# Kernel optimization log

Hardware: AMD Instinct MI355X
Metric: run time of the kernel (lower is better)

The kernel has to match this reference:

```python
import jax, jax.numpy as jnp
import numpy as np

B, IC, H, W = 1024, 3, 32, 32
E, NC = 8, 100            # num_experts, num_classes
GCH, ECH = 16, 32         # gate hidden channels, expert hidden channels
K = 3                     # conv kernel size


def _conv2d(x, w):
    # x: [B,Cin,H,W], w: [Cout,Cin,kh,kw] -> [B,Cout,H,W] (SAME padding, stride 1)
    return jax.lax.conv_general_dilated(
        x, w, window_strides=(1, 1), padding='SAME',
        dimension_numbers=('NCHW', 'OIHW', 'NCHW'))


def setup_inputs() -> dict:
    key = jax.random.key(0)
    ks = jax.random.split(key, 9)
    init = lambda k, shape, fan: (jax.random.normal(k, shape, jnp.float32)
                                  * np.float32(1.0 / np.sqrt(fan)))
    return {
        'x': jax.random.normal(ks[0], (B, IC, H, W), jnp.float32),
        # GatingNetwork: conv(3->16) + relu + global-avg-pool + linear(16->E) + softmax
        'gate_conv_w': init(ks[1], (GCH, IC, K, K), IC * K * K),
        'gate_conv_b': jnp.zeros((GCH,), jnp.float32),
        'gate_lin_w': init(ks[2], (E, GCH), GCH),
        'gate_lin_b': jnp.zeros((E,), jnp.float32),
        # ExpertLayer (per expert): conv(3->32) + relu + global-avg-pool + linear(32->NC)
        'exp_conv_w': init(ks[3], (E, ECH, IC, K, K), IC * K * K),
        'exp_conv_b': jnp.zeros((E, ECH), jnp.float32),
        'exp_lin_w': init(ks[4], (E, NC, ECH), ECH),
        'exp_lin_b': jnp.zeros((E, NC), jnp.float32),
    }


def reference(x, gate_conv_w, gate_conv_b, gate_lin_w, gate_lin_b,
              exp_conv_w, exp_conv_b, exp_lin_w, exp_lin_b):
    # ---- Router: softmax gate over experts ----
    g = jax.nn.relu(_conv2d(x, gate_conv_w) + gate_conv_b[None, :, None, None])
    g = g.mean(axis=(2, 3))                                   # [B,GCH]
    weights = jax.nn.softmax(g @ gate_lin_w.T + gate_lin_b, axis=1)  # [B,E]
    best = jnp.argmax(weights, axis=1)                        # [B] hard top-1

    # ---- All experts as one fused conv (dense compute, then hard select) ----
    e, ch, ic, kh, kw = exp_conv_w.shape
    w_all = exp_conv_w.reshape(e * ch, ic, kh, kw)
    feat = _conv2d(x, w_all)                                  # [B,E*ECH,H,W]
    feat = feat.reshape(x.shape[0], e, ch, feat.shape[2], feat.shape[3])
    feat = jax.nn.relu(feat + exp_conv_b[None, :, :, None, None])
    pooled = feat.mean(axis=(3, 4))                           # [B,E,ECH]
    out_all = jnp.einsum('bec,enc->ben', pooled, exp_lin_w) + exp_lin_b[None]  # [B,E,NC]

    # Combine: each row gets only its argmax expert's output (others -> zero grad)
    final = jnp.take_along_axis(out_all, best[:, None, None], axis=1)[:, 0, :]  # [B,NC]
    return (final, weights)
```

## Files before the change

kernel.cpp:

```cpp
#include <hip/hip_runtime.h>
#include <math.h>

#define NB 1024
#define IC 3
#define HW 32
#define GCH 16
#define ECH 32
#define NE 8
#define NC 100

#define RS 38
#define PS 1292
#define NTX 3876

typedef __attribute__((ext_vector_type(8))) short bf16x8;
typedef __attribute__((ext_vector_type(4))) int   int4v;
typedef __attribute__((ext_vector_type(4))) float f32x4;

__device__ inline short f2bf(float f) {
    unsigned u = __float_as_uint(f);
    unsigned r = (u + 0x7FFF + ((u >> 16) & 1)) >> 16;
    return (short)r;
}
__device__ inline float bf2f(short h) {
    return __uint_as_float(((unsigned)(unsigned short)h) << 16);
}

__global__ __launch_bounds__(256) void moe_fused_kernel(
    const float* __restrict__ x,
    const float* __restrict__ gcw,
    const float* __restrict__ gcb,
    const float* __restrict__ glw,
    const float* __restrict__ glb,
    const float* __restrict__ ecw,
    const float* __restrict__ ecb,
    const float* __restrict__ elw,
    const float* __restrict__ elb,
    float* __restrict__ out_final,
    float* __restrict__ out_w)
{
    __shared__ __align__(16) int xil[NTX];
    __shared__ float red2[4][32];
    __shared__ float pg[GCH];
    __shared__ float pe[ECH];
    __shared__ int s_best;

    const int t = threadIdx.x;
    const int b = blockIdx.x;
    const int lane = t & 63;
    const int wid = t >> 6;
    const int r15 = lane & 15;
    const int kg = lane >> 4;

    for (int i = t; i < NTX / 4; i += 256) ((int4*)xil)[i] = make_int4(0, 0, 0, 0);

    bf16x8 gbh, gbl;
    #pragma unroll
    for (int r = 0; r < 8; ++r) {
        int k = kg * 8 + r;
        float w = (k < 27) ? gcw[r15 * 27 + k] : 0.f;
        short h = f2bf(w);
        gbh[r] = h;
        gbl[r] = f2bf(w - bf2f(h));
    }
    const float gb = gcb[r15];

    __syncthreads();

    const float* xb = x + (size_t)b * (IC * HW * HW);
    #pragma unroll
    for (int i3 = 0; i3 < 3; ++i3) {
        int i = t + i3 * 256;
        float4 v = ((const float4*)xb)[i];
        int ci = i >> 8, rem = i & 255, row = rem >> 3, x4 = (rem & 7) << 2;
        int T = ci * PS + (row + 1) * RS + x4 + 2;
        short h0 = f2bf(v.x), h1 = f2bf(v.y), h2 = f2bf(v.z), h3 = f2bf(v.w);
        int t0 = (unsigned short)h0 | ((unsigned)(unsigned short)f2bf(v.x - bf2f(h0)) << 16);
        int t1 = (unsigned short)h1 | ((unsigned)(unsigned short)f2bf(v.y - bf2f(h1)) << 16);
        int t2 = (unsigned short)h2 | ((unsigned)(unsigned short)f2bf(v.z - bf2f(h2)) << 16);
        int t3 = (unsigned short)h3 | ((unsigned)(unsigned short)f2bf(v.w - bf2f(h3)) << 16);
        *(int2*)&xil[T]     = make_int2(t0, t1);
        *(int2*)&xil[T + 2] = make_int2(t2, t3);
    }

    int off[8];
    #pragma unroll
    for (int r = 0; r < 8; ++r) {
        int k = kg * 8 + r;
        int ci = (k < 27) ? (k / 9) : 0;
        int r9 = (k < 27) ? (k - 9 * ci) : 0;
        int ky = r9 / 3;
        int kx = r9 - 3 * ky;
        off[r] = (k < 27) ? (ci * PS + ky * RS + kx + 1) : 0;
    }

    __syncthreads();

    float sg = 0.f;
    #pragma unroll 2
    for (int m = 0; m < 16; ++m) {
        int px = (wid << 8) + (m << 4) + r15;
        int base = (px >> 5) * RS + (px & 31);
        int T0 = xil[base + off[0]], T1 = xil[base + off[1]];
        int T2 = xil[base + off[2]], T3 = xil[base + off[3]];
        int T4 = xil[base + off[4]], T5 = xil[base + off[5]];
        int T6 = xil[base + off[6]], T7 = xil[base + off[7]];
        int4v ahd = { (int)__builtin_amdgcn_perm(T1, T0, 0x05040100u),
                      (int)__builtin_amdgcn_perm(T3, T2, 0x05040100u),
                      (int)__builtin_amdgcn_perm(T5, T4, 0x05040100u),
                      (int)__builtin_amdgcn_perm(T7, T6, 0x05040100u) };
        int4v ald = { (int)__builtin_amdgcn_perm(T1, T0, 0x07060302u),
                      (int)__builtin_amdgcn_perm(T3, T2, 0x07060302u),
                      (int)__builtin_amdgcn_perm(T5, T4, 0x07060302u),
                      (int)__builtin_amdgcn_perm(T7, T6, 0x07060302u) };
        bf16x8 ah = __builtin_bit_cast(bf16x8, ahd);
        bf16x8 al = __builtin_bit_cast(bf16x8, ald);
        f32x4 d = {0.f, 0.f, 0.f, 0.f};
        d = __builtin_amdgcn_mfma_f32_16x16x32_bf16(al, gbh, d, 0, 0, 0);
        d = __builtin_amdgcn_mfma_f32_16x16x32_bf16(ah, gbl, d, 0, 0, 0);
        d = __builtin_amdgcn_mfma_f32_16x16x32_bf16(ah, gbh, d, 0, 0, 0);
        sg += fmaxf(d[0] + gb, 0.f) + fmaxf(d[1] + gb, 0.f) +
              fmaxf(d[2] + gb, 0.f) + fmaxf(d[3] + gb, 0.f);
    }
    {
        float v = sg;
        v += __shfl_xor(v, 16);
        v += __shfl_xor(v, 32);
        if (lane < 16) red2[wid][lane] = v;
    }
    __syncthreads();
    if (t < GCH)
        pg[t] = (red2[0][t] + red2[1][t] + red2[2][t] + red2[3][t]) * (1.f / 1024.f);
    __syncthreads();

    if (t < NE) {
        float acc = glb[t];
        #pragma unroll
        for (int c = 0; c < GCH; ++c) acc += pg[c] * glw[t * GCH + c];
        float m = acc;
        #pragma unroll
        for (int o = 1; o < NE; o <<= 1) m = fmaxf(m, __shfl_xor(m, o));
        float ex = expf(acc - m);
        float s = ex;
        #pragma unroll
        for (int o = 1; o < NE; o <<= 1) s += __shfl_xor(s, o);
        out_w[(size_t)b * NE + t] = ex / s;
        float mv = acc; int mi = t;
        #pragma unroll
        for (int o = 1; o < NE; o <<= 1) {
            float ov = __shfl_xor(mv, o);
            int   oi = __shfl_xor(mi, o);
            if (ov > mv || (ov == mv && oi < mi)) { mv = ov; mi = oi; }
        }
        if (t == 0) s_best = mi;
    }
    __syncthreads();
    const int e = __builtin_amdgcn_readfirstlane(s_best);

    const float* ewp = ecw + (size_t)e * (ECH * 27);
    const float* ebp = ecb + (size_t)e * ECH;

    bf16x8 bfr0, bfr1;
    #pragma unroll
    for (int r = 0; r < 8; ++r) {
        int k = kg * 8 + r;
        bfr0[r] = f2bf((k < 27) ? ewp[r15 * 27 + k] : 0.f);
        bfr1[r] = f2bf((k < 27) ? ewp[(16 + r15) * 27 + k] : 0.f);
    }
    const float b0 = ebp[r15];
    const float b1 = ebp[16 + r15];

    const short* xs16 = (const short*)xil;
    float s0 = 0.f, s1 = 0.f;
    #pragma unroll 2
    for (int m = 0; m < 16; ++m) {
        int px = (wid << 8) + (m << 4) + r15;
        int base = (px >> 5) * RS + (px & 31);
        bf16x8 a;
        #pragma unroll
        for (int r = 0; r < 8; ++r)
            a[r] = xs16[2 * (base + off[r])];
        f32x4 z = {0.f, 0.f, 0.f, 0.f};
        f32x4 d0 = __builtin_amdgcn_mfma_f32_16x16x32_bf16(a, bfr0, z, 0, 0, 0);
        f32x4 d1 = __builtin_amdgcn_mfma_f32_16x16x32_bf16(a, bfr1, z, 0, 0, 0);
        s0 += fmaxf(d0[0] + b0, 0.f) + fmaxf(d0[1] + b0, 0.f) +
              fmaxf(d0[2] + b0, 0.f) + fmaxf(d0[3] + b0, 0.f);
        s1 += fmaxf(d1[0] + b1, 0.f) + fmaxf(d1[1] + b1, 0.f) +
              fmaxf(d1[2] + b1, 0.f) + fmaxf(d1[3] + b1, 0.f);
    }
    {
        float v0 = s0, v1 = s1;
        v0 += __shfl_xor(v0, 16); v0 += __shfl_xor(v0, 32);
        v1 += __shfl_xor(v1, 16); v1 += __shfl_xor(v1, 32);
        if (lane < 16) { red2[wid][lane] = v0; red2[wid][lane + 16] = v1; }
    }
    __syncthreads();
    if (t < ECH)
        pe[t] = (red2[0][t] + red2[1][t] + red2[2][t] + red2[3][t]) * (1.f / 1024.f);
    __syncthreads();

    if (t < NC) {
        const float* lw = elw + ((size_t)e * NC + t) * ECH;
        float acc = elb[e * NC + t];
        #pragma unroll
        for (int c = 0; c < ECH; ++c) acc += pe[c] * lw[c];
        out_final[(size_t)b * NC + t] = acc;
    }
}

extern "C" void kernel_launch(void* const* d_in, const int* in_sizes, int n_in,
                              void* d_out, int out_size, void* d_ws, size_t ws_size,
                              hipStream_t stream) {
    const float* x   = (const float*)d_in[0];
    const float* gcw = (const float*)d_in[1];
    const float* gcb = (const float*)d_in[2];
    const float* glw = (const float*)d_in[3];
    const float* glb = (const float*)d_in[4];
    const float* ecw = (const float*)d_in[5];
    const float* ecb = (const float*)d_in[6];
    const float* elw = (const float*)d_in[7];
    const float* elb = (const float*)d_in[8];

    float* out_final = (float*)d_out;
    float* out_w     = (float*)d_out + NB * NC;

    hipLaunchKernelGGL(moe_fused_kernel, dim3(NB), dim3(256), 0, stream,
                       x, gcw, gcb, glw, glb, ecw, ecb, elw, elb,
                       out_final, out_w);
}
```

Before: 19.89 us.

## Interleave channels per row in LDS and remap K-slices to fixed tap offsets

```diff
diff --git a/kernel.cpp b/kernel.cpp
--- a/kernel.cpp
+++ b/kernel.cpp
@@ -9,8 +9,8 @@
 #define NE 8
 #define NC 100
 
-#define RS 38
-#define PS 1292
+#define CS 38
+#define RS2 114
 #define NTX 3876
 
 typedef __attribute__((ext_vector_type(8))) short bf16x8;
@@ -51,14 +51,17 @@
     const int wid = t >> 6;
     const int r15 = lane & 15;
     const int kg = lane >> 4;
+    const bool k3 = (kg == 3);
+    const int kgoff = k3 ? 0 : kg * CS;
 
     for (int i = t; i < NTX / 4; i += 256) ((int4*)xil)[i] = make_int4(0, 0, 0, 0);
 
     bf16x8 gbh, gbl;
     #pragma unroll
     for (int r = 0; r < 8; ++r) {
-        int k = kg * 8 + r;
-        float w = (k < 27) ? gcw[r15 * 27 + k] : 0.f;
+        float w = 0.f;
+        if (kg < 3) w = gcw[r15 * 27 + kg * 9 + r];
+        else if (r < 3) w = gcw[r15 * 27 + r * 9 + 8];
         short h = f2bf(w);
         gbh[r] = h;
         gbl[r] = f2bf(w - bf2f(h));
@@ -73,7 +76,7 @@
         int i = t + i3 * 256;
         float4 v = ((const float4*)xb)[i];
         int ci = i >> 8, rem = i & 255, row = rem >> 3, x4 = (rem & 7) << 2;
-        int T = ci * PS + (row + 1) * RS + x4 + 2;
+        int T = (row + 1) * RS2 + ci * CS + x4 + 2;
         short h0 = f2bf(v.x), h1 = f2bf(v.y), h2 = f2bf(v.z), h3 = f2bf(v.w);
         int t0 = (unsigned short)h0 | ((unsigned)(unsigned short)f2bf(v.x - bf2f(h0)) << 16);
         int t1 = (unsigned short)h1 | ((unsigned)(unsigned short)f2bf(v.y - bf2f(h1)) << 16);
@@ -83,34 +86,30 @@
         *(int2*)&xil[T + 2] = make_int2(t2, t3);
     }
 
-    int off[8];
-    #pragma unroll
-    for (int r = 0; r < 8; ++r) {
-        int k = kg * 8 + r;
-        int ci = (k < 27) ? (k / 9) : 0;
-        int r9 = (k < 27) ? (k - 9 * ci) : 0;
-        int ky = r9 / 3;
-        int kx = r9 - 3 * ky;
-        off[r] = (k < 27) ? (ci * PS + ky * RS + kx + 1) : 0;
-    }
-
     __syncthreads();
 
     float sg = 0.f;
     #pragma unroll 2
     for (int m = 0; m < 16; ++m) {
         int px = (wid << 8) + (m << 4) + r15;
-        int base = (px >> 5) * RS + (px & 31);
-        int T0 = xil[base + off[0]], T1 = xil[base + off[1]];
-        int T2 = xil[base + off[2]], T3 = xil[base + off[3]];
-        int T4 = xil[base + off[4]], T5 = xil[base + off[5]];
-        int T6 = xil[base + off[6]], T7 = xil[base + off[7]];
-        int4v ahd = { (int)__builtin_amdgcn_perm(T1, T0, 0x05040100u),
-                      (int)__builtin_amdgcn_perm(T3, T2, 0x05040100u),
+        int rowbase = (px >> 5) * RS2 + (px & 31) + 1;
+        int vA = rowbase + kgoff;
+        int vB = rowbase + 2 * RS2;
+        int T0 = xil[vA];           int T1 = xil[vA + 1];
+        int T2 = xil[vA + 2];       int T3 = xil[vA + RS2];
+        int T4 = xil[vA + RS2 + 1]; int T5 = xil[vA + RS2 + 2];
+        int T6 = xil[vA + 2 * RS2]; int T7 = xil[vA + 2 * RS2 + 1];
+        int U0 = xil[vB + 2];       int U1 = xil[vB + 2 + CS];
+        int U2 = xil[vB + 2 + 2 * CS];
+        int X0 = k3 ? U0 : T0;
+        int X1 = k3 ? U1 : T1;
+        int X2 = k3 ? U2 : T2;
+        int4v ahd = { (int)__builtin_amdgcn_perm(X1, X0, 0x05040100u),
+                      (int)__builtin_amdgcn_perm(T3, X2, 0x05040100u),
                       (int)__builtin_amdgcn_perm(T5, T4, 0x05040100u),
                       (int)__builtin_amdgcn_perm(T7, T6, 0x05040100u) };
-        int4v ald = { (int)__builtin_amdgcn_perm(T1, T0, 0x07060302u),
-                      (int)__builtin_amdgcn_perm(T3, T2, 0x07060302u),
+        int4v ald = { (int)__builtin_amdgcn_perm(X1, X0, 0x07060302u),
+                      (int)__builtin_amdgcn_perm(T3, X2, 0x07060302u),
                       (int)__builtin_amdgcn_perm(T5, T4, 0x07060302u),
                       (int)__builtin_amdgcn_perm(T7, T6, 0x07060302u) };
         bf16x8 ah = __builtin_bit_cast(bf16x8, ahd);
@@ -163,23 +162,41 @@
     bf16x8 bfr0, bfr1;
     #pragma unroll
     for (int r = 0; r < 8; ++r) {
-        int k = kg * 8 + r;
-        bfr0[r] = f2bf((k < 27) ? ewp[r15 * 27 + k] : 0.f);
-        bfr1[r] = f2bf((k < 27) ? ewp[(16 + r15) * 27 + k] : 0.f);
+        float w0 = 0.f, w1 = 0.f;
+        if (kg < 3) {
+            w0 = ewp[r15 * 27 + kg * 9 + r];
+            w1 = ewp[(16 + r15) * 27 + kg * 9 + r];
+        } else if (r < 3) {
+            w0 = ewp[r15 * 27 + r * 9 + 8];
+            w1 = ewp[(16 + r15) * 27 + r * 9 + 8];
+        }
+        bfr0[r] = f2bf(w0);
+        bfr1[r] = f2bf(w1);
     }
     const float b0 = ebp[r15];
     const float b1 = ebp[16 + r15];
 
-    const short* xs16 = (const short*)xil;
     float s0 = 0.f, s1 = 0.f;
     #pragma unroll 2
     for (int m = 0; m < 16; ++m) {
         int px = (wid << 8) + (m << 4) + r15;
-        int base = (px >> 5) * RS + (px & 31);
-        bf16x8 a;
-        #pragma unroll
-        for (int r = 0; r < 8; ++r)
-            a[r] = xs16[2 * (base + off[r])];
+        int rowbase = (px >> 5) * RS2 + (px & 31) + 1;
+        int vA = rowbase + kgoff;
+        int vB = rowbase + 2 * RS2;
+        int T0 = xil[vA];           int T1 = xil[vA + 1];
+        int T2 = xil[vA + 2];       int T3 = xil[vA + RS2];
+        int T4 = xil[vA + RS2 + 1]; int T5 = xil[vA + RS2 + 2];
+        int T6 = xil[vA + 2 * RS2]; int T7 = xil[vA + 2 * RS2 + 1];
+        int U0 = xil[vB + 2];       int U1 = xil[vB + 2 + CS];
+        int U2 = xil[vB + 2 + 2 * CS];
+        int X0 = k3 ? U0 : T0;
+        int X1 = k3 ? U1 : T1;
+        int X2 = k3 ? U2 : T2;
+        int4v ahd = { (int)__builtin_amdgcn_perm(X1, X0, 0x05040100u),
+                      (int)__builtin_amdgcn_perm(T3, X2, 0x05040100u),
+                      (int)__builtin_amdgcn_perm(T5, T4, 0x05040100u),
+                      (int)__builtin_amdgcn_perm(T7, T6, 0x05040100u) };
+        bf16x8 a = __builtin_bit_cast(bf16x8, ahd);
         f32x4 z = {0.f, 0.f, 0.f, 0.f};
         f32x4 d0 = __builtin_amdgcn_mfma_f32_16x16x32_bf16(a, bfr0, z, 0, 0, 0);
         f32x4 d1 = __builtin_amdgcn_mfma_f32_16x16x32_bf16(a, bfr1, z, 0, 0, 0);
```

Result: no change. 19.83 us (median of 3 runs) (-0.3%).
